# Kernel tuning notes

Hardware: AMD Instinct MI355X
Metric: run time of the kernel (lower is better)

The kernel has to match this reference:

```python
import jax, jax.numpy as jnp
import numpy as np

HEADS = 4
DIM_HEAD = 64
DIM = 256
FMAP = 64
SCALE = DIM_HEAD ** -0.5


def setup_inputs() -> dict:
    key = jax.random.key(0)
    k1, k2, k3, k4 = jax.random.split(key, 4)
    inner = HEADS * DIM_HEAD
    fmap = jax.random.normal(k1, (4, DIM, FMAP, FMAP), dtype=jnp.float32)
    # 1x1 conv weight for qkv projection: (3*inner_dim, dim)
    w_qkv = jax.random.normal(k2, (3 * inner, DIM), dtype=jnp.float32) * (DIM ** -0.5)
    # AbsPosEmb parameters, initialized as randn * dim_head**-0.5 (as in BoTNet)
    pos_height = jax.random.normal(k3, (FMAP, DIM_HEAD), dtype=jnp.float32) * SCALE
    pos_width = jax.random.normal(k4, (FMAP, DIM_HEAD), dtype=jnp.float32) * SCALE
    return {"fmap": fmap, "w_qkv": w_qkv, "pos_height": pos_height, "pos_width": pos_width}


def reference(fmap, w_qkv, pos_height, pos_width):
    b, c, h, w = fmap.shape
    hw = h * w
    # 1x1 conv (no bias) == channel matmul
    qkv = jnp.einsum('bchw,oc->bohw', fmap, w_qkv)  # (b, 3*inner, h, w)
    q, k, v = jnp.split(qkv, 3, axis=1)
    # replicate torch .view(b, heads, h*w, -1): raw row-major reshape
    q = q.reshape(b, HEADS, hw, DIM_HEAD) * SCALE
    k = k.reshape(b, HEADS, hw, DIM_HEAD)
    v = v.reshape(b, HEADS, hw, DIM_HEAD)
    sim = jnp.einsum('bhid,bhjd->bhij', q, k)  # (b, heads, hw, hw)
    # absolute positional bias: emb[j] = height[y] + width[x], j = y*w + x
    emb = (pos_height[:, None, :] + pos_width[None, :, :]).reshape(hw, DIM_HEAD)
    sim = sim + jnp.einsum('bhid,jd->bhij', q, emb)
    attn = jax.nn.softmax(sim, axis=-1)
    out = jnp.einsum('bhij,bhjd->bhid', attn, v)  # (b, heads, hw, dim_head)
    # replicate torch .view(b, heads*dim_head, h, w): raw reshape
    return out.reshape(b, HEADS * DIM_HEAD, h, w)
```

## Files before the change

### kernel.cpp

```cpp
#include <hip/hip_runtime.h>


typedef float  f32x4  __attribute__((ext_vector_type(4)));
typedef __bf16 bf16x8 __attribute__((ext_vector_type(8)));
typedef __bf16 bf16x4 __attribute__((ext_vector_type(4)));

__device__ inline float fast_exp2(float x) {
#if __has_builtin(__builtin_amdgcn_exp2f)
  return __builtin_amdgcn_exp2f(x);
#else
  return exp2f(x);
#endif
}

__device__ inline void glds16(const __bf16* g, __bf16* l) {
  __builtin_amdgcn_global_load_lds(
      (const __attribute__((address_space(1))) void*)g,
      (__attribute__((address_space(3))) void*)l, 16, 0, 0);
}

__global__ __launch_bounds__(256) void w_cvt(
    const float* __restrict__ w, __bf16* __restrict__ wb)
{
  int idx = blockIdx.x * 256 + threadIdx.x;
  f32x4 v = ((const f32x4*)w)[idx];
  bf16x4 o; o[0]=(__bf16)v[0]; o[1]=(__bf16)v[1]; o[2]=(__bf16)v[2]; o[3]=(__bf16)v[3];
  ((bf16x4*)wb)[idx] = o;
}

__global__ __launch_bounds__(256) void qkv_proj(
    const float* __restrict__ fmap, const __bf16* __restrict__ wb,
    const float* __restrict__ ph,   const float* __restrict__ pw,
    __bf16* __restrict__ Qw, __bf16* __restrict__ Kw, __bf16* __restrict__ Vw)
{
  constexpr int LS = 264;
  __shared__ __bf16 Bs[32 * LS];
  const int tid  = threadIdx.x;
  const int wv   = tid >> 6;
  const int lane = tid & 63;
  const int quad = lane >> 4, l15 = lane & 15;
  const int n0 = blockIdx.x * 32;
  const int b  = blockIdx.y;

#pragma unroll
  for (int i = 0; i < 2; ++i) {
    int id = tid + i * 256;
    int ng = id & 7;
    int kg = id >> 3;
    const float* base = fmap + ((size_t)b * 256 + 4 * kg) * 4096 + n0 + 4 * ng;
    f32x4 v0 = *(const f32x4*)(base);
    f32x4 v1 = *(const f32x4*)(base + 4096);
    f32x4 v2 = *(const f32x4*)(base + 8192);
    f32x4 v3 = *(const f32x4*)(base + 12288);
#pragma unroll
    for (int j = 0; j < 4; ++j) {
      bf16x4 o; o[0]=(__bf16)v0[j]; o[1]=(__bf16)v1[j]; o[2]=(__bf16)v2[j]; o[3]=(__bf16)v3[j];
      *(bf16x4*)(&Bs[(4 * ng + j) * LS + 4 * kg]) = o;
    }
  }
  __syncthreads();

  for (int mt = 0; mt < 12; ++mt) {
    const int region = mt >> 2;
    const int obase  = (mt & 3) * 64;
    const __bf16* aptr = wb + (size_t)(mt * 64 + 16 * wv + l15) * 256 + 8 * quad;

    f32x4 acc[2] = {};
#pragma unroll
    for (int k0 = 0; k0 < 256; k0 += 32) {
      bf16x8 af = *(const bf16x8*)(aptr + k0);
      bf16x8 b0 = *(const bf16x8*)(&Bs[(l15)      * LS + k0 + 8 * quad]);
      bf16x8 b1 = *(const bf16x8*)(&Bs[(16 + l15) * LS + k0 + 8 * quad]);
      acc[0] = __builtin_amdgcn_mfma_f32_16x16x32_bf16(af, b0, acc[0], 0, 0, 0);
      acc[1] = __builtin_amdgcn_mfma_f32_16x16x32_bf16(af, b1, acc[1], 0, 0, 0);
    }

#pragma unroll
    for (int t = 0; t < 2; ++t) {
#pragma unroll
      for (int rr = 0; rr < 4; ++rr) {
        int oreg = obase + 16 * wv + 4 * quad + rr;
        int s    = n0 + 16 * t + l15;
        float val = acc[t][rr];
        size_t off = ((size_t)(b * 256 + oreg)) * 4096 + s;
        if (region == 0) {
          Qw[off] = (__bf16)(val * 0.18033688f);
        } else if (region == 1) {
          int g = oreg & 63;
          float bias = ph[g * 64 + (s & 63)] + pw[(s >> 6) * 64 + (s & 63)];
          Kw[off] = (__bf16)(val + bias);
        } else {
          Vw[off] = (__bf16)val;
        }
      }
    }
  }
}

__global__ __launch_bounds__(256) void v_transpose(
    const __bf16* __restrict__ Vw, __bf16* __restrict__ Vt)
{
  __shared__ __bf16 T[64 * 72];
  const int tid = threadIdx.x;
  const int j0  = blockIdx.x * 64;
  const int bh  = blockIdx.y;
  const __bf16* src = Vw + (size_t)bh * 262144;
#pragma unroll
  for (int i = 0; i < 2; ++i) {
    int id = tid + i * 256;
    int r = id >> 3, c = (id & 7) * 8;
    *(bf16x8*)(&T[r * 72 + c]) = *(const bf16x8*)(src + (size_t)(j0 + r) * 64 + c);
  }
  __syncthreads();
#pragma unroll
  for (int i = 0; i < 2; ++i) {
    int id = tid + i * 256;
    int d = id >> 3, jc = (id & 7) * 8;
    bf16x8 o;
#pragma unroll
    for (int z = 0; z < 8; ++z) o[z] = T[(jc + z) * 72 + d];
    *(bf16x8*)(Vt + ((size_t)bh * 64 + d) * 4096 + j0 + jc) = o;
  }
}

__global__ __launch_bounds__(512, 2) void flash_attn(
    const __bf16* __restrict__ Qg, const __bf16* __restrict__ Kg,
    const __bf16* __restrict__ Vtg, float* __restrict__ out)
{
  __shared__ __align__(16) __bf16 SMEM[65536];
  __bf16* Ks = SMEM;
  __bf16* Vs = SMEM + 32768;

  const int tid  = threadIdx.x;
  const int wv   = tid >> 6;
  const int lane = tid & 63;
  const int quad = lane >> 4, l15 = lane & 15;
  const int zi   = wv >> 2;
  const int wl   = wv & 3;
  const int l   = blockIdx.y * 16 + blockIdx.x;
  const int bh  = 2 * (l & 7) + ((l >> 3) & 1);
  const int ibx = l >> 4;
  const int iw = ibx * 256 + 64 * wl;
  const __bf16* Qb = Qg  + (size_t)bh * 262144;
  const __bf16* Kb = Kg  + (size_t)bh * 262144;
  const __bf16* Vb = Vtg + (size_t)bh * 262144;

  bf16x8 qf[4][2];
#pragma unroll
  for (int m = 0; m < 4; ++m)
#pragma unroll
    for (int c = 0; c < 2; ++c)
      qf[m][c] = *(const bf16x8*)(Qb + (size_t)(iw + 16 * m + l15) * 64 + 32 * c + 8 * quad);

  const int r0  = tid >> 3;
  const int kch = tid & 7;
  const int xc  = (kch ^ (r0 & 7)) * 8;
  const int prr = (r0 & 0x23) | ((r0 & 0x0C) << 1) | ((r0 & 0x10) >> 2);
  const __bf16* kp0 = Kb + (size_t)prr * 64 + xc;
  const __bf16* kp1 = Kb + (size_t)(2048 + prr) * 64 + xc;
  const __bf16* vp0 = Vb + (size_t)r0 * 4096 + xc;
  const __bf16* vp1 = Vb + (size_t)r0 * 4096 + 2048 + xc;

  f32x4 acco[4][4] = {};
  f32x4 lacc[4] = {};
  const int swz = (l15 & 7);

  bf16x8 onesb;
#pragma unroll
  for (int r = 0; r < 8; ++r) onesb[r] = (__bf16)1.0f;

  auto dma_tile = [&](int buf) {
    __bf16* kd0 = &Ks[buf * 8192 + tid * 8];
    __bf16* kd1 = &Ks[16384 + buf * 8192 + tid * 8];
    __bf16* vd0 = &Vs[buf * 8192 + tid * 8];
    __bf16* vd1 = &Vs[16384 + buf * 8192 + tid * 8];
    glds16(kp0, kd0);         kp0 += 4096;
    glds16(kp0, kd0 + 4096);  kp0 += 4096;
    glds16(kp1, kd1);         kp1 += 4096;
    glds16(kp1, kd1 + 4096);  kp1 += 4096;
    glds16(vp0, vd0);         vp0 += 64;
    glds16(vp0, vd0 + 4096);  vp0 += 64;
    glds16(vp1, vd1);         vp1 += 64;
    glds16(vp1, vd1 + 4096);  vp1 += 64;
  };

  auto compute_tile = [&](int buf, int sub) {
    const __bf16* Kbuf = &Ks[zi * 16384 + buf * 8192 + sub * 4096];
    const __bf16* Vbuf = &Vs[zi * 16384 + buf * 8192 + sub * 4096];
    f32x4 sacc[4][4] = {};
    __builtin_amdgcn_s_setprio(1);
#pragma unroll
    for (int c = 0; c < 2; ++c) {
#pragma unroll
      for (int t = 0; t < 4; ++t) {
        bf16x8 ak = *(const bf16x8*)(&Kbuf[(16 * t + l15) * 64 + (((4 * c + quad) ^ swz) * 8)]);
#pragma unroll
        for (int m = 0; m < 4; ++m)
          sacc[m][t] = __builtin_amdgcn_mfma_f32_16x16x32_bf16(ak, qf[m][c], sacc[m][t], 0, 0, 0);
      }
    }
    __builtin_amdgcn_s_setprio(0);
    bf16x8 pf[4][2];
#pragma unroll
    for (int m = 0; m < 4; ++m) {
#pragma unroll
      for (int t = 0; t < 4; ++t)
#pragma unroll
        for (int r = 0; r < 4; ++r)
          sacc[m][t][r] = fast_exp2(sacc[m][t][r]);
#pragma unroll
      for (int c2 = 0; c2 < 2; ++c2) {
        bf16x8 a;
#pragma unroll
        for (int r = 0; r < 4; ++r) {
          a[r]     = (__bf16)sacc[m][2 * c2][r];
          a[4 + r] = (__bf16)sacc[m][2 * c2 + 1][r];
        }
        pf[m][c2] = a;
      }
    }
    __builtin_amdgcn_s_setprio(1);
#pragma unroll
    for (int c2 = 0; c2 < 2; ++c2) {
#pragma unroll
      for (int t = 0; t < 4; ++t) {
        bf16x8 bv = *(const bf16x8*)(&Vbuf[(16 * t + l15) * 64 + (((4 * c2 + quad) ^ swz) * 8)]);
#pragma unroll
        for (int m = 0; m < 4; ++m)
          acco[m][t] = __builtin_amdgcn_mfma_f32_16x16x32_bf16(pf[m][c2], bv, acco[m][t], 0, 0, 0);
      }
#pragma unroll
      for (int m = 0; m < 4; ++m)
        lacc[m] = __builtin_amdgcn_mfma_f32_16x16x32_bf16(pf[m][c2], onesb, lacc[m], 0, 0, 0);
    }
    __builtin_amdgcn_s_setprio(0);
  };

  dma_tile(0);
  for (int it = 0; it < 16; it += 2) {
    __syncthreads();
    dma_tile(1);
    compute_tile(0, 0);
    compute_tile(0, 1);
    __syncthreads();
    if (it < 14) dma_tile(0);
    compute_tile(1, 0);
    compute_tile(1, 1);
  }

  __syncthreads();
  float* X = (float*)SMEM;
  const int slot = (wl * 64 + lane) * 84;
  if (zi == 1) {
#pragma unroll
    for (int m = 0; m < 4; ++m) {
#pragma unroll
      for (int t = 0; t < 4; ++t)
        *(f32x4*)(&X[slot + m * 16 + t * 4]) = acco[m][t];
      *(f32x4*)(&X[slot + 64 + m * 4]) = lacc[m];
    }
  }
  __syncthreads();
  if (zi == 0) {
    float* Ob = out + (size_t)bh * 262144;
#pragma unroll
    for (int m = 0; m < 4; ++m) {
      f32x4 l1 = *(const f32x4*)(&X[slot + 64 + m * 4]);
      f32x4 lt = lacc[m] + l1;
      f32x4 inv;
#pragma unroll
      for (int r = 0; r < 4; ++r) inv[r] = 1.0f / lt[r];
#pragma unroll
      for (int t = 0; t < 4; ++t) {
        f32x4 o1 = *(const f32x4*)(&X[slot + m * 16 + t * 4]);
        f32x4 ot = acco[m][t] + o1;
#pragma unroll
        for (int r = 0; r < 4; ++r)
          Ob[(size_t)(iw + 16 * m + 4 * quad + r) * 64 + 16 * t + l15] =
              ot[r] * inv[r];
      }
    }
  }
}

extern "C" void kernel_launch(void* const* d_in, const int* in_sizes, int n_in,
                              void* d_out, int out_size, void* d_ws, size_t ws_size,
                              hipStream_t stream) {
  const float* fmap = (const float*)d_in[0];
  const float* w    = (const float*)d_in[1];
  const float* ph   = (const float*)d_in[2];
  const float* pw   = (const float*)d_in[3];
  float* out = (float*)d_out;

  __bf16* Qw = (__bf16*)d_ws;
  __bf16* Kw = Qw + 4194304;
  __bf16* Vw = Kw + 4194304;
  __bf16* Vt = Vw + 4194304;
  __bf16* Wb16 = (__bf16*)(Vt + 4194304);

  w_cvt      <<<dim3(192),    256, 0, stream>>>(w, Wb16);
  qkv_proj   <<<dim3(128, 4), 256, 0, stream>>>(fmap, Wb16, ph, pw, Qw, Kw, Vw);
  v_transpose<<<dim3(64, 16), 256, 0, stream>>>(Vw, Vt);
  flash_attn <<<dim3(16, 16), 512, 0, stream>>>(Qw, Kw, Vt, out);
}
```

Before: 174.3 us.

## Drop key-split across wave groups; each wave owns 32 query rows

The flash attention kernel no longer splits the key range between two groups of four waves that are merged through shared memory at the end. Each of the eight waves now handles 32 query rows over the full 4096 keys, so shared memory shrinks to 64 KB and the launch bound asks for four blocks per CU. This removes the final LDS reduction and its barriers and halves per-wave register use. In exchange, each K/V tile loaded into LDS is reused by fewer query rows per MFMA (2 m-blocks instead of 4), and the loop runs twice as many iterations with twice as many barriers.

Result: slower. 178.6 us (+2.4%).

```diff
diff --git a/kernel.cpp b/kernel.cpp
--- a/kernel.cpp
+++ b/kernel.cpp
@@ -123,31 +123,28 @@
   }
 }
 
-__global__ __launch_bounds__(512, 2) void flash_attn(
+__global__ __launch_bounds__(512, 4) void flash_attn(
     const __bf16* __restrict__ Qg, const __bf16* __restrict__ Kg,
     const __bf16* __restrict__ Vtg, float* __restrict__ out)
 {
-  __shared__ __align__(16) __bf16 SMEM[65536];
-  __bf16* Ks = SMEM;
-  __bf16* Vs = SMEM + 32768;
+  __shared__ __align__(16) __bf16 Ks[16384];
+  __shared__ __align__(16) __bf16 Vs[16384];
 
   const int tid  = threadIdx.x;
   const int wv   = tid >> 6;
   const int lane = tid & 63;
   const int quad = lane >> 4, l15 = lane & 15;
-  const int zi   = wv >> 2;
-  const int wl   = wv & 3;
   const int l   = blockIdx.y * 16 + blockIdx.x;
   const int bh  = 2 * (l & 7) + ((l >> 3) & 1);
   const int ibx = l >> 4;
-  const int iw = ibx * 256 + 64 * wl;
+  const int iw  = ibx * 256 + 32 * wv;
   const __bf16* Qb = Qg  + (size_t)bh * 262144;
   const __bf16* Kb = Kg  + (size_t)bh * 262144;
   const __bf16* Vb = Vtg + (size_t)bh * 262144;
 
-  bf16x8 qf[4][2];
-#pragma unroll
-  for (int m = 0; m < 4; ++m)
+  bf16x8 qf[2][2];
+#pragma unroll
+  for (int m = 0; m < 2; ++m)
 #pragma unroll
     for (int c = 0; c < 2; ++c)
       qf[m][c] = *(const bf16x8*)(Qb + (size_t)(iw + 16 * m + l15) * 64 + 32 * c + 8 * quad);
@@ -156,13 +153,11 @@
   const int kch = tid & 7;
   const int xc  = (kch ^ (r0 & 7)) * 8;
   const int prr = (r0 & 0x23) | ((r0 & 0x0C) << 1) | ((r0 & 0x10) >> 2);
-  const __bf16* kp0 = Kb + (size_t)prr * 64 + xc;
-  const __bf16* kp1 = Kb + (size_t)(2048 + prr) * 64 + xc;
-  const __bf16* vp0 = Vb + (size_t)r0 * 4096 + xc;
-  const __bf16* vp1 = Vb + (size_t)r0 * 4096 + 2048 + xc;
-
-  f32x4 acco[4][4] = {};
-  f32x4 lacc[4] = {};
+  const __bf16* kp = Kb + (size_t)prr * 64 + xc;
+  const __bf16* vp = Vb + (size_t)r0 * 4096 + xc;
+
+  f32x4 acco[2][4] = {};
+  f32x4 lacc[2] = {};
   const int swz = (l15 & 7);
 
   bf16x8 onesb;
@@ -170,24 +165,18 @@
   for (int r = 0; r < 8; ++r) onesb[r] = (__bf16)1.0f;
 
   auto dma_tile = [&](int buf) {
-    __bf16* kd0 = &Ks[buf * 8192 + tid * 8];
-    __bf16* kd1 = &Ks[16384 + buf * 8192 + tid * 8];
-    __bf16* vd0 = &Vs[buf * 8192 + tid * 8];
-    __bf16* vd1 = &Vs[16384 + buf * 8192 + tid * 8];
-    glds16(kp0, kd0);         kp0 += 4096;
-    glds16(kp0, kd0 + 4096);  kp0 += 4096;
-    glds16(kp1, kd1);         kp1 += 4096;
-    glds16(kp1, kd1 + 4096);  kp1 += 4096;
-    glds16(vp0, vd0);         vp0 += 64;
-    glds16(vp0, vd0 + 4096);  vp0 += 64;
-    glds16(vp1, vd1);         vp1 += 64;
-    glds16(vp1, vd1 + 4096);  vp1 += 64;
+    __bf16* kd = &Ks[buf * 8192 + tid * 8];
+    __bf16* vd = &Vs[buf * 8192 + tid * 8];
+    glds16(kp, kd);         kp += 4096;
+    glds16(kp, kd + 4096);  kp += 4096;
+    glds16(vp, vd);         vp += 64;
+    glds16(vp, vd + 4096);  vp += 64;
   };
 
   auto compute_tile = [&](int buf, int sub) {
-    const __bf16* Kbuf = &Ks[zi * 16384 + buf * 8192 + sub * 4096];
-    const __bf16* Vbuf = &Vs[zi * 16384 + buf * 8192 + sub * 4096];
-    f32x4 sacc[4][4] = {};
+    const __bf16* Kbuf = &Ks[buf * 8192 + sub * 4096];
+    const __bf16* Vbuf = &Vs[buf * 8192 + sub * 4096];
+    f32x4 sacc[2][4] = {};
     __builtin_amdgcn_s_setprio(1);
 #pragma unroll
     for (int c = 0; c < 2; ++c) {
@@ -195,14 +184,14 @@
       for (int t = 0; t < 4; ++t) {
         bf16x8 ak = *(const bf16x8*)(&Kbuf[(16 * t + l15) * 64 + (((4 * c + quad) ^ swz) * 8)]);
 #pragma unroll
-        for (int m = 0; m < 4; ++m)
+        for (int m = 0; m < 2; ++m)
           sacc[m][t] = __builtin_amdgcn_mfma_f32_16x16x32_bf16(ak, qf[m][c], sacc[m][t], 0, 0, 0);
       }
     }
     __builtin_amdgcn_s_setprio(0);
-    bf16x8 pf[4][2];
-#pragma unroll
-    for (int m = 0; m < 4; ++m) {
+    bf16x8 pf[2][2];
+#pragma unroll
+    for (int m = 0; m < 2; ++m) {
 #pragma unroll
       for (int t = 0; t < 4; ++t)
 #pragma unroll
@@ -226,60 +215,40 @@
       for (int t = 0; t < 4; ++t) {
         bf16x8 bv = *(const bf16x8*)(&Vbuf[(16 * t + l15) * 64 + (((4 * c2 + quad) ^ swz) * 8)]);
 #pragma unroll
-        for (int m = 0; m < 4; ++m)
+        for (int m = 0; m < 2; ++m)
           acco[m][t] = __builtin_amdgcn_mfma_f32_16x16x32_bf16(pf[m][c2], bv, acco[m][t], 0, 0, 0);
       }
 #pragma unroll
-      for (int m = 0; m < 4; ++m)
+      for (int m = 0; m < 2; ++m)
         lacc[m] = __builtin_amdgcn_mfma_f32_16x16x32_bf16(pf[m][c2], onesb, lacc[m], 0, 0, 0);
     }
     __builtin_amdgcn_s_setprio(0);
   };
 
   dma_tile(0);
-  for (int it = 0; it < 16; it += 2) {
+  for (int it = 0; it < 32; it += 2) {
     __syncthreads();
     dma_tile(1);
     compute_tile(0, 0);
     compute_tile(0, 1);
     __syncthreads();
-    if (it < 14) dma_tile(0);
+    if (it < 30) dma_tile(0);
     compute_tile(1, 0);
     compute_tile(1, 1);
   }
 
-  __syncthreads();
-  float* X = (float*)SMEM;
-  const int slot = (wl * 64 + lane) * 84;
-  if (zi == 1) {
-#pragma unroll
-    for (int m = 0; m < 4; ++m) {
-#pragma unroll
-      for (int t = 0; t < 4; ++t)
-        *(f32x4*)(&X[slot + m * 16 + t * 4]) = acco[m][t];
-      *(f32x4*)(&X[slot + 64 + m * 4]) = lacc[m];
-    }
-  }
-  __syncthreads();
-  if (zi == 0) {
-    float* Ob = out + (size_t)bh * 262144;
-#pragma unroll
-    for (int m = 0; m < 4; ++m) {
-      f32x4 l1 = *(const f32x4*)(&X[slot + 64 + m * 4]);
-      f32x4 lt = lacc[m] + l1;
-      f32x4 inv;
-#pragma unroll
-      for (int r = 0; r < 4; ++r) inv[r] = 1.0f / lt[r];
-#pragma unroll
-      for (int t = 0; t < 4; ++t) {
-        f32x4 o1 = *(const f32x4*)(&X[slot + m * 16 + t * 4]);
-        f32x4 ot = acco[m][t] + o1;
-#pragma unroll
-        for (int r = 0; r < 4; ++r)
-          Ob[(size_t)(iw + 16 * m + 4 * quad + r) * 64 + 16 * t + l15] =
-              ot[r] * inv[r];
-      }
-    }
+  float* Ob = out + (size_t)bh * 262144;
+#pragma unroll
+  for (int m = 0; m < 2; ++m) {
+    f32x4 inv;
+#pragma unroll
+    for (int r = 0; r < 4; ++r) inv[r] = 1.0f / lacc[m][r];
+#pragma unroll
+    for (int t = 0; t < 4; ++t)
+#pragma unroll
+      for (int r = 0; r < 4; ++r)
+        Ob[(size_t)(iw + 16 * m + 4 * quad + r) * 64 + 16 * t + l15] =
+            acco[m][t][r] * inv[r];
   }
 }
 
```
